# Kernel tuning notes

Hardware: AMD Instinct MI355X
Metric: run time of the kernel (lower is better)

Reference implementation:

```python
import jax, jax.numpy as jnp
import numpy as np

EMBED_DIM = 128
D3 = EMBED_DIM // 3  # 42
K = 3  # k = min(3, N-1); N >> 4 so k is statically 3


def _local_density(points):
    # points: [B, N, 3] -> mean distance to 3 nearest neighbors, [B, N, 1]
    sq = jnp.sum(points * points, axis=-1)  # [B, N]
    d2 = sq[:, :, None] + sq[:, None, :] - 2.0 * jnp.einsum('bnd,bmd->bnm', points, points)
    dists = jnp.sqrt(jnp.maximum(d2, 1e-12))  # [B, N, N]
    N = points.shape[1]
    eye = jnp.eye(N, dtype=bool)
    dists = jnp.where(eye[None, :, :], jnp.inf, dists)
    # k smallest = -(k largest of negated)
    neg_topk, _ = jax.lax.top_k(-dists, K)  # [B, N, K]
    return jnp.mean(-neg_topk, axis=-1, keepdims=True)  # [B, N, 1]


def setup_inputs() -> dict:
    key = jax.random.key(0)
    ks = jax.random.split(key, 9)
    B, N = 8, 4096
    points = jax.random.normal(ks[0], (B, N, 3), dtype=jnp.float32)
    # PyTorch Linear init scale: U(-1/sqrt(fan_in), 1/sqrt(fan_in))
    def lin(k, fan_in, fan_out):
        k1, k2 = jax.random.split(k)
        bnd = 1.0 / np.sqrt(fan_in)
        W = jax.random.uniform(k1, (fan_in, fan_out), jnp.float32, -bnd, bnd)
        b = jax.random.uniform(k2, (fan_out,), jnp.float32, -bnd, bnd)
        return W, b
    W_rel, b_rel = lin(ks[1], 3, D3)
    W_dist, b_dist = lin(ks[2], 1, D3)
    W_dens, b_dens = lin(ks[3], 1, D3)
    W_out, b_out = lin(ks[4], 3 * D3, EMBED_DIM)
    return {"points": points, "W_rel": W_rel, "b_rel": b_rel,
            "W_dist": W_dist, "b_dist": b_dist, "W_dens": W_dens, "b_dens": b_dens,
            "W_out": W_out, "b_out": b_out}


def reference(points, W_rel, b_rel, W_dist, b_dist, W_dens, b_dens, W_out, b_out):
    centroid = jnp.mean(points, axis=1, keepdims=True)          # [B, 1, 3]
    relative_pos = points - centroid                             # [B, N, 3]
    rel_features = relative_pos @ W_rel + b_rel                  # [B, N, D3]
    centroid_dist = jnp.linalg.norm(relative_pos, axis=-1, keepdims=True)  # [B, N, 1]
    dist_features = centroid_dist @ W_dist + b_dist              # [B, N, D3]
    local_density = _local_density(points)                       # [B, N, 1]
    density_features = local_density @ W_dens + b_dens           # [B, N, D3]
    features = jnp.concatenate([rel_features, dist_features, density_features], axis=-1)
    return features @ W_out + b_out                              # [B, N, 128]
```

## Files before the change

kernel.cpp:

```cpp
#include <hip/hip_runtime.h>
#include <math.h>

#define NPTS 4096
#define NBATCH 8

#define INS3(t0, t1, t2, v)                                   \
    {                                                         \
        float n0 = fminf(t0, (v));                            \
        float n1 = __builtin_amdgcn_fmed3f(t0, t1, (v));      \
        float n2 = __builtin_amdgcn_fmed3f(t1, t2, (v));      \
        t0 = n0; t1 = n1; t2 = n2;                            \
    }

#define MERGE3(t0, t1, t2, m)                                 \
    {                                                         \
        float b0 = __shfl_xor(t0, m);                         \
        float b1 = __shfl_xor(t1, m);                         \
        float b2 = __shfl_xor(t2, m);                         \
        float X = fmaxf(t0, b0);                              \
        t0 = fminf(t0, b0);                                   \
        float Y = fminf(t1, b1);                              \
        float Z = fmaxf(X, Y);                                \
        t1 = fminf(X, Y);                                     \
        t2 = fminf(Z, fminf(t2, b2));                         \
    }

#define RFL(x) __uint_as_float(__builtin_amdgcn_readfirstlane(__float_as_uint(x)))

#define DECLQ(j)                                              \
    float4 Q##j = lp4[qb + j];                                \
    float qx##j = RFL(-2.0f * Q##j.x);                        \
    float qy##j = RFL(-2.0f * Q##j.y);                        \
    float qz##j = RFL(-2.0f * Q##j.z);                        \
    float sq##j = RFL(Q##j.w);                                \
    float t##j##0 = INFINITY, t##j##1 = INFINITY, t##j##2 = INFINITY;

#define STEP(j)                                                             \
    {                                                                       \
        float e = fmaf(qx##j, c.x, fmaf(qy##j, c.y, fmaf(qz##j, c.z, c.w)));\
        INS3(t##j##0, t##j##1, t##j##2, e);                                 \
    }

#define SELF(j)                                                             \
    if (lane == (((w << 3) + j) & 63)) {                                    \
        t##j##0 = t##j##1; t##j##1 = t##j##2; t##j##2 = INFINITY;           \
    }

#define MRG(j, m) MERGE3(t##j##0, t##j##1, t##j##2, m)

#define DENS(j)                                                             \
    float d##j = (sqrtf(fmaxf(t##j##0 + sq##j, 1e-12f)) +                   \
                  sqrtf(fmaxf(t##j##1 + sq##j, 1e-12f)) +                   \
                  sqrtf(fmaxf(t##j##2 + sq##j, 1e-12f))) * (1.0f / 3.0f);

__launch_bounds__(1024, 4)
__global__ void fused_kernel(const float* __restrict__ pts,
                             const float* __restrict__ W_rel, const float* __restrict__ b_rel,
                             const float* __restrict__ W_dist, const float* __restrict__ b_dist,
                             const float* __restrict__ W_dens, const float* __restrict__ b_dens,
                             const float* __restrict__ W_out, const float* __restrict__ b_out,
                             float* __restrict__ out) {
    __shared__ float4 lp4[NPTS];
    __shared__ float4 cpart[16];
    __shared__ float4 cent;
    __shared__ __align__(16) float Clds[6][128];
    __shared__ float dens[128];

    int b = blockIdx.x >> 5;
    int g = blockIdx.x & 31;
    int tid = threadIdx.x;
    int w = tid >> 6, lane = tid & 63;

    {
        const float4* P4 = (const float4*)(pts + (size_t)b * NPTS * 3);
        float4 v0 = P4[3 * tid + 0];
        float4 v1 = P4[3 * tid + 1];
        float4 v2 = P4[3 * tid + 2];
        float x0 = v0.x, y0 = v0.y, z0 = v0.z;
        float x1 = v0.w, y1 = v1.x, z1 = v1.y;
        float x2 = v1.z, y2 = v1.w, z2 = v2.x;
        float x3 = v2.y, y3 = v2.z, z3 = v2.w;
        lp4[4 * tid + 0] = make_float4(x0, y0, z0, fmaf(x0, x0, fmaf(y0, y0, z0 * z0)));
        lp4[4 * tid + 1] = make_float4(x1, y1, z1, fmaf(x1, x1, fmaf(y1, y1, z1 * z1)));
        lp4[4 * tid + 2] = make_float4(x2, y2, z2, fmaf(x2, x2, fmaf(y2, y2, z2 * z2)));
        lp4[4 * tid + 3] = make_float4(x3, y3, z3, fmaf(x3, x3, fmaf(y3, y3, z3 * z3)));
        float sx = (x0 + x1) + (x2 + x3);
        float sy = (y0 + y1) + (y2 + y3);
        float sz = (z0 + z1) + (z2 + z3);
        #pragma unroll
        for (int m = 1; m < 64; m <<= 1) {
            sx += __shfl_xor(sx, m);
            sy += __shfl_xor(sy, m);
            sz += __shfl_xor(sz, m);
        }
        if (lane == 0) cpart[w] = make_float4(sx, sy, sz, 0.f);
    }
    __syncthreads();

    if (w == 0 && lane < 16) {
        float4 p = cpart[lane];
        float cx = p.x, cy = p.y, cz = p.z;
        #pragma unroll
        for (int m = 1; m < 16; m <<= 1) {
            cx += __shfl_xor(cx, m);
            cy += __shfl_xor(cy, m);
            cz += __shfl_xor(cz, m);
        }
        if (lane == 0) {
            const float inv = 1.0f / (float)NPTS;
            cent = make_float4(cx * inv, cy * inv, cz * inv, 0.f);
        }
    }
    if (tid < 128) {
        int o = tid;
        float a0 = 0.f, a1 = 0.f, a2 = 0.f, vd = 0.f, vl = 0.f, be = b_out[o];
        for (int j = 0; j < 42; ++j) {
            float w0 = W_out[j * 128 + o];
            float w1 = W_out[(42 + j) * 128 + o];
            float w2 = W_out[(84 + j) * 128 + o];
            a0 = fmaf(W_rel[j],      w0, a0);
            a1 = fmaf(W_rel[42 + j], w0, a1);
            a2 = fmaf(W_rel[84 + j], w0, a2);
            vd = fmaf(W_dist[j],     w1, vd);
            vl = fmaf(W_dens[j],     w2, vl);
            be = fmaf(b_rel[j],  w0, be);
            be = fmaf(b_dist[j], w1, be);
            be = fmaf(b_dens[j], w2, be);
        }
        Clds[0][o] = a0; Clds[1][o] = a1; Clds[2][o] = a2;
        Clds[3][o] = vd; Clds[4][o] = vl; Clds[5][o] = be;
    }

    int qb = (g << 7) + (w << 3);
    DECLQ(0) DECLQ(1) DECLQ(2) DECLQ(3) DECLQ(4) DECLQ(5) DECLQ(6) DECLQ(7)

    #pragma unroll 4
    for (int tile = 0; tile < 64; ++tile) {
        float4 c = lp4[(tile << 6) + lane];
        STEP(0) STEP(1) STEP(2) STEP(3) STEP(4) STEP(5) STEP(6) STEP(7)
    }

    SELF(0) SELF(1) SELF(2) SELF(3) SELF(4) SELF(5) SELF(6) SELF(7)

    #pragma unroll
    for (int m = 1; m < 64; m <<= 1) {
        MRG(0, m) MRG(1, m) MRG(2, m) MRG(3, m)
        MRG(4, m) MRG(5, m) MRG(6, m) MRG(7, m)
    }

    DENS(0) DENS(1) DENS(2) DENS(3) DENS(4) DENS(5) DENS(6) DENS(7)
    if (lane == 0) {
        int db = w << 3;
        dens[db + 0] = d0; dens[db + 1] = d1; dens[db + 2] = d2; dens[db + 3] = d3;
        dens[db + 4] = d4; dens[db + 5] = d5; dens[db + 6] = d6; dens[db + 7] = d7;
    }
    __syncthreads();

    {
        int r = tid >> 3;
        int c16 = (tid & 7) << 4;
        float4 p = lp4[(g << 7) + r];
        float rx = p.x - cent.x, ry = p.y - cent.y, rz = p.z - cent.z;
        float cd = sqrtf(fmaf(rx, rx, fmaf(ry, ry, rz * rz)));
        float ld = dens[r];
        float* orow = out + ((size_t)(b * NPTS + (g << 7) + r)) * 128;
        #pragma unroll
        for (int h = 0; h < 4; ++h) {
            int o = c16 + 4 * h;
            float4 A0 = *(const float4*)&Clds[0][o];
            float4 A1 = *(const float4*)&Clds[1][o];
            float4 A2 = *(const float4*)&Clds[2][o];
            float4 VD = *(const float4*)&Clds[3][o];
            float4 VL = *(const float4*)&Clds[4][o];
            float4 BE = *(const float4*)&Clds[5][o];
            float4 rv;
            rv.x = fmaf(rx, A0.x, fmaf(ry, A1.x, fmaf(rz, A2.x, fmaf(cd, VD.x, fmaf(ld, VL.x, BE.x)))));
            rv.y = fmaf(rx, A0.y, fmaf(ry, A1.y, fmaf(rz, A2.y, fmaf(cd, VD.y, fmaf(ld, VL.y, BE.y)))));
            rv.z = fmaf(rx, A0.z, fmaf(ry, A1.z, fmaf(rz, A2.z, fmaf(cd, VD.z, fmaf(ld, VL.z, BE.z)))));
            rv.w = fmaf(rx, A0.w, fmaf(ry, A1.w, fmaf(rz, A2.w, fmaf(cd, VD.w, fmaf(ld, VL.w, BE.w)))));
            *(float4*)(orow + o) = rv;
        }
    }
}

extern "C" void kernel_launch(void* const* d_in, const int* in_sizes, int n_in,
                              void* d_out, int out_size, void* d_ws, size_t ws_size,
                              hipStream_t stream) {
    const float* pts    = (const float*)d_in[0];
    const float* W_rel  = (const float*)d_in[1];
    const float* b_rel  = (const float*)d_in[2];
    const float* W_dist = (const float*)d_in[3];
    const float* b_dist = (const float*)d_in[4];
    const float* W_dens = (const float*)d_in[5];
    const float* b_dens = (const float*)d_in[6];
    const float* W_out  = (const float*)d_in[7];
    const float* b_out  = (const float*)d_in[8];
    float* out = (float*)d_out;

    hipLaunchKernelGGL(fused_kernel, dim3(NBATCH * 32), dim3(1024), 0, stream,
                       pts, W_rel, b_rel, W_dist, b_dist, W_dens, b_dens, W_out, b_out, out);
}
```

Baseline: 39.94 us.

## Split centroid/coefficient prep into separate kernel and halve density block size

Result: slower. 43.42 us (+8.7%).

```diff
diff --git a/kernel.cpp b/kernel.cpp
--- a/kernel.cpp
+++ b/kernel.cpp
@@ -4,115 +4,44 @@
 #define NPTS 4096
 #define NBATCH 8
 
-#define INS3(t0, t1, t2, v)                                   \
-    {                                                         \
-        float n0 = fminf(t0, (v));                            \
-        float n1 = __builtin_amdgcn_fmed3f(t0, t1, (v));      \
-        float n2 = __builtin_amdgcn_fmed3f(t1, t2, (v));      \
-        t0 = n0; t1 = n1; t2 = n2;                            \
-    }
-
-#define MERGE3(t0, t1, t2, m)                                 \
-    {                                                         \
-        float b0 = __shfl_xor(t0, m);                         \
-        float b1 = __shfl_xor(t1, m);                         \
-        float b2 = __shfl_xor(t2, m);                         \
-        float X = fmaxf(t0, b0);                              \
-        t0 = fminf(t0, b0);                                   \
-        float Y = fminf(t1, b1);                              \
-        float Z = fmaxf(X, Y);                                \
-        t1 = fminf(X, Y);                                     \
-        t2 = fminf(Z, fminf(t2, b2));                         \
-    }
-
-#define RFL(x) __uint_as_float(__builtin_amdgcn_readfirstlane(__float_as_uint(x)))
-
-#define DECLQ(j)                                              \
-    float4 Q##j = lp4[qb + j];                                \
-    float qx##j = RFL(-2.0f * Q##j.x);                        \
-    float qy##j = RFL(-2.0f * Q##j.y);                        \
-    float qz##j = RFL(-2.0f * Q##j.z);                        \
-    float sq##j = RFL(Q##j.w);                                \
-    float t##j##0 = INFINITY, t##j##1 = INFINITY, t##j##2 = INFINITY;
-
-#define STEP(j)                                                             \
-    {                                                                       \
-        float e = fmaf(qx##j, c.x, fmaf(qy##j, c.y, fmaf(qz##j, c.z, c.w)));\
-        INS3(t##j##0, t##j##1, t##j##2, e);                                 \
-    }
-
-#define SELF(j)                                                             \
-    if (lane == (((w << 3) + j) & 63)) {                                    \
-        t##j##0 = t##j##1; t##j##1 = t##j##2; t##j##2 = INFINITY;           \
-    }
-
-#define MRG(j, m) MERGE3(t##j##0, t##j##1, t##j##2, m)
-
-#define DENS(j)                                                             \
-    float d##j = (sqrtf(fmaxf(t##j##0 + sq##j, 1e-12f)) +                   \
-                  sqrtf(fmaxf(t##j##1 + sq##j, 1e-12f)) +                   \
-                  sqrtf(fmaxf(t##j##2 + sq##j, 1e-12f))) * (1.0f / 3.0f);
-
-__launch_bounds__(1024, 4)
-__global__ void fused_kernel(const float* __restrict__ pts,
-                             const float* __restrict__ W_rel, const float* __restrict__ b_rel,
-                             const float* __restrict__ W_dist, const float* __restrict__ b_dist,
-                             const float* __restrict__ W_dens, const float* __restrict__ b_dens,
-                             const float* __restrict__ W_out, const float* __restrict__ b_out,
-                             float* __restrict__ out) {
-    __shared__ float4 lp4[NPTS];
-    __shared__ float4 cpart[16];
-    __shared__ float4 cent;
-    __shared__ __align__(16) float Clds[6][128];
-    __shared__ float dens[128];
-
-    int b = blockIdx.x >> 5;
-    int g = blockIdx.x & 31;
-    int tid = threadIdx.x;
-    int w = tid >> 6, lane = tid & 63;
-
-    {
-        const float4* P4 = (const float4*)(pts + (size_t)b * NPTS * 3);
-        float4 v0 = P4[3 * tid + 0];
-        float4 v1 = P4[3 * tid + 1];
-        float4 v2 = P4[3 * tid + 2];
-        float x0 = v0.x, y0 = v0.y, z0 = v0.z;
-        float x1 = v0.w, y1 = v1.x, z1 = v1.y;
-        float x2 = v1.z, y2 = v1.w, z2 = v2.x;
-        float x3 = v2.y, y3 = v2.z, z3 = v2.w;
-        lp4[4 * tid + 0] = make_float4(x0, y0, z0, fmaf(x0, x0, fmaf(y0, y0, z0 * z0)));
-        lp4[4 * tid + 1] = make_float4(x1, y1, z1, fmaf(x1, x1, fmaf(y1, y1, z1 * z1)));
-        lp4[4 * tid + 2] = make_float4(x2, y2, z2, fmaf(x2, x2, fmaf(y2, y2, z2 * z2)));
-        lp4[4 * tid + 3] = make_float4(x3, y3, z3, fmaf(x3, x3, fmaf(y3, y3, z3 * z3)));
-        float sx = (x0 + x1) + (x2 + x3);
-        float sy = (y0 + y1) + (y2 + y3);
-        float sz = (z0 + z1) + (z2 + z3);
-        #pragma unroll
-        for (int m = 1; m < 64; m <<= 1) {
-            sx += __shfl_xor(sx, m);
-            sy += __shfl_xor(sy, m);
-            sz += __shfl_xor(sz, m);
-        }
-        if (lane == 0) cpart[w] = make_float4(sx, sy, sz, 0.f);
-    }
-    __syncthreads();
-
-    if (w == 0 && lane < 16) {
-        float4 p = cpart[lane];
-        float cx = p.x, cy = p.y, cz = p.z;
-        #pragma unroll
-        for (int m = 1; m < 16; m <<= 1) {
-            cx += __shfl_xor(cx, m);
-            cy += __shfl_xor(cy, m);
-            cz += __shfl_xor(cz, m);
-        }
-        if (lane == 0) {
+#define WS_CENT 0
+#define WS_COEF 32
+
+__launch_bounds__(256)
+__global__ void prep_kernel(const float* __restrict__ pts,
+                            const float* __restrict__ W_rel, const float* __restrict__ b_rel,
+                            const float* __restrict__ W_dist, const float* __restrict__ b_dist,
+                            const float* __restrict__ W_dens, const float* __restrict__ b_dens,
+                            const float* __restrict__ W_out, const float* __restrict__ b_out,
+                            float* __restrict__ ws) {
+    __shared__ float sx[256], sy[256], sz[256];
+    if (blockIdx.x < NBATCH) {
+        int b = blockIdx.x;
+        const float* P = pts + (size_t)b * NPTS * 3;
+        float ax = 0.f, ay = 0.f, az = 0.f;
+        for (int n = threadIdx.x; n < NPTS; n += 256) {
+            ax += P[3 * n + 0];
+            ay += P[3 * n + 1];
+            az += P[3 * n + 2];
+        }
+        sx[threadIdx.x] = ax; sy[threadIdx.x] = ay; sz[threadIdx.x] = az;
+        __syncthreads();
+        for (int off = 128; off > 0; off >>= 1) {
+            if (threadIdx.x < off) {
+                sx[threadIdx.x] += sx[threadIdx.x + off];
+                sy[threadIdx.x] += sy[threadIdx.x + off];
+                sz[threadIdx.x] += sz[threadIdx.x + off];
+            }
+            __syncthreads();
+        }
+        if (threadIdx.x == 0) {
             const float inv = 1.0f / (float)NPTS;
-            cent = make_float4(cx * inv, cy * inv, cz * inv, 0.f);
-        }
-    }
-    if (tid < 128) {
-        int o = tid;
+            ws[WS_CENT + 4 * b + 0] = sx[0] * inv;
+            ws[WS_CENT + 4 * b + 1] = sy[0] * inv;
+            ws[WS_CENT + 4 * b + 2] = sz[0] * inv;
+        }
+    } else if (threadIdx.x < 128) {
+        int o = threadIdx.x;
         float a0 = 0.f, a1 = 0.f, a2 = 0.f, vd = 0.f, vl = 0.f, be = b_out[o];
         for (int j = 0; j < 42; ++j) {
             float w0 = W_out[j * 128 + o];
@@ -127,16 +56,100 @@
             be = fmaf(b_dist[j], w1, be);
             be = fmaf(b_dens[j], w2, be);
         }
-        Clds[0][o] = a0; Clds[1][o] = a1; Clds[2][o] = a2;
-        Clds[3][o] = vd; Clds[4][o] = vl; Clds[5][o] = be;
-    }
-
-    int qb = (g << 7) + (w << 3);
+        float* C = ws + WS_COEF;
+        C[0 * 128 + o] = a0; C[1 * 128 + o] = a1; C[2 * 128 + o] = a2;
+        C[3 * 128 + o] = vd; C[4 * 128 + o] = vl; C[5 * 128 + o] = be;
+    }
+}
+
+#define INS3(t0, t1, t2, v)                                   \
+    {                                                         \
+        float n0 = fminf(t0, (v));                            \
+        float n1 = __builtin_amdgcn_fmed3f(t0, t1, (v));      \
+        float n2 = __builtin_amdgcn_fmed3f(t1, t2, (v));      \
+        t0 = n0; t1 = n1; t2 = n2;                            \
+    }
+
+#define MERGE3(t0, t1, t2, m)                                 \
+    {                                                         \
+        float b0 = __shfl_xor(t0, m);                         \
+        float b1 = __shfl_xor(t1, m);                         \
+        float b2 = __shfl_xor(t2, m);                         \
+        float X = fmaxf(t0, b0);                              \
+        t0 = fminf(t0, b0);                                   \
+        float Y = fminf(t1, b1);                              \
+        float Z = fmaxf(X, Y);                                \
+        t1 = fminf(X, Y);                                     \
+        t2 = fminf(Z, fminf(t2, b2));                         \
+    }
+
+#define RFL(x) __uint_as_float(__builtin_amdgcn_readfirstlane(__float_as_uint(x)))
+
+#define DECLQ(j)                                              \
+    float4 Q##j = lp4s[j][qrow];                              \
+    float qx##j = RFL(-2.0f * Q##j.x);                        \
+    float qy##j = RFL(-2.0f * Q##j.y);                        \
+    float qz##j = RFL(-2.0f * Q##j.z);                        \
+    float sq##j = RFL(Q##j.w);                                \
+    float t##j##0 = INFINITY, t##j##1 = INFINITY, t##j##2 = INFINITY;
+
+#define STEP(j)                                                             \
+    {                                                                       \
+        float e = fmaf(qx##j, c.x, fmaf(qy##j, c.y, fmaf(qz##j, c.z, c.w)));\
+        INS3(t##j##0, t##j##1, t##j##2, e);                                 \
+    }
+
+#define SELF(j)                                                             \
+    if (lane == ((w << 3) + j)) {                                           \
+        t##j##0 = t##j##1; t##j##1 = t##j##2; t##j##2 = INFINITY;           \
+    }
+
+#define MRG(j, m) MERGE3(t##j##0, t##j##1, t##j##2, m)
+
+#define DENS(j)                                                             \
+    float d##j = (sqrtf(fmaxf(t##j##0 + sq##j, 1e-12f)) +                   \
+                  sqrtf(fmaxf(t##j##1 + sq##j, 1e-12f)) +                   \
+                  sqrtf(fmaxf(t##j##2 + sq##j, 1e-12f))) * (1.0f / 3.0f);
+
+__launch_bounds__(512, 4)
+__global__ void density_out_kernel(const float* __restrict__ pts,
+                                   const float* __restrict__ ws,
+                                   float* __restrict__ out) {
+    __shared__ float4 lp4s[8][513];
+    __shared__ float dens[64];
+    int b = blockIdx.x >> 6;
+    int g = blockIdx.x & 63;
+    int tid = threadIdx.x;
+    int w = tid >> 6, lane = tid & 63;
+
+    {
+        const float4* P4 = (const float4*)(pts + (size_t)b * NPTS * 3);
+        float4 v0 = P4[6 * tid + 0];
+        float4 v1 = P4[6 * tid + 1];
+        float4 v2 = P4[6 * tid + 2];
+        float4 v3 = P4[6 * tid + 3];
+        float4 v4 = P4[6 * tid + 4];
+        float4 v5 = P4[6 * tid + 5];
+        #define SQ4(x, y, z) make_float4((x), (y), (z), fmaf((x), (x), fmaf((y), (y), (z) * (z))))
+        lp4s[0][tid] = SQ4(v0.x, v0.y, v0.z);
+        lp4s[1][tid] = SQ4(v0.w, v1.x, v1.y);
+        lp4s[2][tid] = SQ4(v1.z, v1.w, v2.x);
+        lp4s[3][tid] = SQ4(v2.y, v2.z, v2.w);
+        lp4s[4][tid] = SQ4(v3.x, v3.y, v3.z);
+        lp4s[5][tid] = SQ4(v3.w, v4.x, v4.y);
+        lp4s[6][tid] = SQ4(v4.z, v4.w, v5.x);
+        lp4s[7][tid] = SQ4(v5.y, v5.z, v5.w);
+        #undef SQ4
+    }
+    __syncthreads();
+
+    int qrow = (g << 3) + w;
     DECLQ(0) DECLQ(1) DECLQ(2) DECLQ(3) DECLQ(4) DECLQ(5) DECLQ(6) DECLQ(7)
 
+    const float4* cbase = &lp4s[lane & 7][lane >> 3];
     #pragma unroll 4
     for (int tile = 0; tile < 64; ++tile) {
-        float4 c = lp4[(tile << 6) + lane];
+        float4 c = cbase[tile << 3];
         STEP(0) STEP(1) STEP(2) STEP(3) STEP(4) STEP(5) STEP(6) STEP(7)
     }
 
@@ -158,27 +171,32 @@
 
     {
         int r = tid >> 3;
-        int c16 = (tid & 7) << 4;
-        float4 p = lp4[(g << 7) + r];
-        float rx = p.x - cent.x, ry = p.y - cent.y, rz = p.z - cent.z;
+        int cb = (tid & 7) << 2;
+        int m = (g << 6) + r;
+        float4 p = lp4s[m & 7][m >> 3];
+        float cx = ws[WS_CENT + 4 * b + 0];
+        float cy = ws[WS_CENT + 4 * b + 1];
+        float cz = ws[WS_CENT + 4 * b + 2];
+        float rx = p.x - cx, ry = p.y - cy, rz = p.z - cz;
         float cd = sqrtf(fmaf(rx, rx, fmaf(ry, ry, rz * rz)));
         float ld = dens[r];
-        float* orow = out + ((size_t)(b * NPTS + (g << 7) + r)) * 128;
+        const float4* Cg = (const float4*)(ws + WS_COEF);
+        float4* orow = (float4*)(out + ((size_t)b * NPTS + m) * 128);
         #pragma unroll
         for (int h = 0; h < 4; ++h) {
-            int o = c16 + 4 * h;
-            float4 A0 = *(const float4*)&Clds[0][o];
-            float4 A1 = *(const float4*)&Clds[1][o];
-            float4 A2 = *(const float4*)&Clds[2][o];
-            float4 VD = *(const float4*)&Clds[3][o];
-            float4 VL = *(const float4*)&Clds[4][o];
-            float4 BE = *(const float4*)&Clds[5][o];
+            int ob = cb + h;
+            float4 A0 = Cg[0 * 32 + ob];
+            float4 A1 = Cg[1 * 32 + ob];
+            float4 A2 = Cg[2 * 32 + ob];
+            float4 VD = Cg[3 * 32 + ob];
+            float4 VL = Cg[4 * 32 + ob];
+            float4 BE = Cg[5 * 32 + ob];
             float4 rv;
             rv.x = fmaf(rx, A0.x, fmaf(ry, A1.x, fmaf(rz, A2.x, fmaf(cd, VD.x, fmaf(ld, VL.x, BE.x)))));
             rv.y = fmaf(rx, A0.y, fmaf(ry, A1.y, fmaf(rz, A2.y, fmaf(cd, VD.y, fmaf(ld, VL.y, BE.y)))));
             rv.z = fmaf(rx, A0.z, fmaf(ry, A1.z, fmaf(rz, A2.z, fmaf(cd, VD.z, fmaf(ld, VL.z, BE.z)))));
             rv.w = fmaf(rx, A0.w, fmaf(ry, A1.w, fmaf(rz, A2.w, fmaf(cd, VD.w, fmaf(ld, VL.w, BE.w)))));
-            *(float4*)(orow + o) = rv;
+            orow[ob] = rv;
         }
     }
 }
@@ -196,7 +214,10 @@
     const float* W_out  = (const float*)d_in[7];
     const float* b_out  = (const float*)d_in[8];
     float* out = (float*)d_out;
-
-    hipLaunchKernelGGL(fused_kernel, dim3(NBATCH * 32), dim3(1024), 0, stream,
-                       pts, W_rel, b_rel, W_dist, b_dist, W_dens, b_dens, W_out, b_out, out);
+    float* ws  = (float*)d_ws;
+
+    hipLaunchKernelGGL(prep_kernel, dim3(NBATCH + 1), dim3(256), 0, stream,
+                       pts, W_rel, b_rel, W_dist, b_dist, W_dens, b_dens, W_out, b_out, ws);
+    hipLaunchKernelGGL(density_out_kernel, dim3(NBATCH * 64), dim3(512), 0, stream,
+                       pts, ws, out);
 }
```
